# Kernel optimization log

Hardware: AMD Instinct MI355X
Metric: run time of the kernel (lower is better)

Reference implementation:

```python
import jax, jax.numpy as jnp
import numpy as np

B, S, D, H = 4, 2048, 1024, 16
HD = D // H  # head_dim = 64


def setup_inputs() -> dict:
    key = jax.random.key(0)
    ks = jax.random.split(key, 4)
    scale = 0.02
    return {
        "x": jax.random.normal(ks[0], (B, S, D), dtype=jnp.float32),
        "W_attn": jax.random.normal(ks[1], (D, 3 * D), dtype=jnp.float32) * scale,
        "b_attn": jnp.zeros((3 * D,), dtype=jnp.float32),
        "W_proj": jax.random.normal(ks[2], (D, D), dtype=jnp.float32) * scale,
        "b_proj": jnp.zeros((D,), dtype=jnp.float32),
    }


def reference(x, W_attn, b_attn, W_proj, b_proj):
    b, s, d = x.shape
    qkv = x @ W_attn + b_attn                      # [b, s, 3d]
    q, k, v = jnp.split(qkv, 3, axis=2)
    # [b, s, d] -> [b, h, s, hd]
    def to_heads(t):
        return t.reshape(b, s, H, HD).transpose(0, 2, 1, 3)
    q, k, v = to_heads(q), to_heads(k), to_heads(v)
    scores = jnp.einsum("bhqd,bhkd->bhqk", q, k) / jnp.sqrt(jnp.float32(HD))
    causal = jnp.tril(jnp.ones((s, s), dtype=bool))  # [s, s]
    scores = jnp.where(causal[None, None], scores, jnp.float32(-jnp.inf))
    probs = jax.nn.softmax(scores, axis=-1)
    y = jnp.einsum("bhqk,bhkd->bhqd", probs, v)    # [b, h, s, hd]
    y = y.transpose(0, 2, 1, 3).reshape(b, s, d)
    return y @ W_proj + b_proj
```

## Files before the change

kernel.cpp:

```cpp
#include <hip/hip_runtime.h>
#include <hip/hip_bf16.h>
#include <type_traits>

#define SQ    2048
#define DIM   1024
#define NH    16
#define HDIM  64
#define BATCH 4

typedef unsigned short u16;
typedef __bf16 bf16x8 __attribute__((ext_vector_type(8)));
typedef float  f32x4  __attribute__((ext_vector_type(4)));
typedef u16    u16x8  __attribute__((ext_vector_type(8)));

#define QSCALE 0.180336880f

__device__ __forceinline__ u16 f2bf(float f) {
  union { float f; unsigned u; } v; v.f = f;
  unsigned r = v.u + 0x7fffu + ((v.u >> 16) & 1u);
  return (u16)(r >> 16);
}

__device__ __forceinline__ float fast_exp2(float x) {
#if __has_builtin(__builtin_amdgcn_exp2f)
  return __builtin_amdgcn_exp2f(x);
#else
  float y;
  asm("v_exp_f32 %0, %1" : "=v"(y) : "v"(x));
  return y;
#endif
}

__device__ __forceinline__ void gll16(const u16* g, u16* l) {
  __builtin_amdgcn_global_load_lds((const __attribute__((address_space(1))) void*)g,
                                   (__attribute__((address_space(3))) void*)l,
                                   16, 0, 0);
}

__global__ __launch_bounds__(256)
void f32_to_bf16_vec(const float* __restrict__ in, u16* __restrict__ out, int n4)
{
  const int i = blockIdx.x * blockDim.x + threadIdx.x;
  if (i < n4) {
    const float4 v = ((const float4*)in)[i];
    ushort4 o;
    o.x = f2bf(v.x); o.y = f2bf(v.y); o.z = f2bf(v.z); o.w = f2bf(v.w);
    ((ushort4*)out)[i] = o;
  }
}

__global__ void transpose_f32_bf16(const float* __restrict__ in, u16* __restrict__ out,
                                   int R, int C)
{
  __shared__ u16 tile[32][33];
  const int bx = blockIdx.x * 32, by = blockIdx.y * 32;
  const int tx = threadIdx.x, ty = threadIdx.y;
  #pragma unroll
  for (int i = 0; i < 32; i += 8)
    tile[ty + i][tx] = f2bf(in[(size_t)(by + ty + i) * C + bx + tx]);
  __syncthreads();
  #pragma unroll
  for (int i = 0; i < 32; i += 8)
    out[(size_t)(bx + ty + i) * R + by + tx] = tile[tx][ty + i];
}

template<int MODE>
__global__ __launch_bounds__(256)
void gemm_bt(const u16* __restrict__ A, const u16* __restrict__ Bt,
             const float* __restrict__ bias, int K,
             u16* __restrict__ o0, u16* __restrict__ o1, float* __restrict__ of)
{
  __shared__ __align__(16) u16 A0[128 * 32], A1[128 * 32];
  __shared__ __align__(16) u16 B0[128 * 32], B1[128 * 32];

  const int t    = threadIdx.x;
  const int lane = t & 63, wave = t >> 6;
  const int l15  = lane & 15, quad = lane >> 4;
  const int wm   = (wave & 1) * 64, wn = (wave >> 1) * 64;
  const int m0   = blockIdx.y * 128, n0 = blockIdx.x * 128;

  const int srow = wave * 32 + (lane >> 2);
  const int scol = (lane & 3) * 8;

  f32x4 acc[4][4] = {};

  for (int k0 = 0; k0 < K; k0 += 64) {
    const u16* ga = A  + (size_t)(m0 + srow) * K + k0 + scol;
    const u16* gb = Bt + (size_t)(n0 + srow) * K + k0 + scol;
    gll16(ga,              &A0[(wave * 32)      * 32]);
    gll16(ga + 32,         &A1[(wave * 32)      * 32]);
    gll16(ga + 16 * K,     &A0[(wave * 32 + 16) * 32]);
    gll16(ga + 16 * K + 32,&A1[(wave * 32 + 16) * 32]);
    gll16(gb,              &B0[(wave * 32)      * 32]);
    gll16(gb + 32,         &B1[(wave * 32)      * 32]);
    gll16(gb + 16 * K,     &B0[(wave * 32 + 16) * 32]);
    gll16(gb + 16 * K + 32,&B1[(wave * 32 + 16) * 32]);
    __syncthreads();

    #pragma unroll
    for (int ks = 0; ks < 2; ++ks) {
      const u16* Als = ks ? A1 : A0;
      const u16* Bls = ks ? B1 : B0;
      bf16x8 af[4], bfr[4];
      #pragma unroll
      for (int i = 0; i < 4; ++i) af[i]  = *(const bf16x8*)&Als[(wm + 16*i + l15) * 32 + quad * 8];
      #pragma unroll
      for (int j = 0; j < 4; ++j) bfr[j] = *(const bf16x8*)&Bls[(wn + 16*j + l15) * 32 + quad * 8];
      #pragma unroll
      for (int i = 0; i < 4; ++i)
        #pragma unroll
        for (int j = 0; j < 4; ++j)
          acc[i][j] = (MODE == 2)
            ? __builtin_amdgcn_mfma_f32_16x16x32_bf16(bfr[j], af[i], acc[i][j], 0, 0, 0)
            : __builtin_amdgcn_mfma_f32_16x16x32_bf16(af[i], bfr[j], acc[i][j], 0, 0, 0);
    }
    __syncthreads();
  }

  if (MODE == 2) {
    #pragma unroll
    for (int j = 0; j < 4; ++j) {
      #pragma unroll
      for (int r = 0; r < 4; ++r) {
        const int d = n0 + wn + 16*j + quad * 4 + r;
        const float bn = bias[d];
        const int h = d >> 6, hd = d & 63;
        #pragma unroll
        for (int i = 0; i < 4; ++i) {
          const int m = m0 + wm + 16*i + l15;
          const int b = m >> 11, s = m & 2047;
          o0[(((size_t)(b * NH + h)) * HDIM + hd) * SQ + s] = f2bf(acc[i][j][r] + bn);
        }
      }
    }
  } else {
    #pragma unroll
    for (int j = 0; j < 4; ++j) {
      const int n = n0 + wn + 16*j + l15;
      const float bn = bias[n];
      #pragma unroll
      for (int i = 0; i < 4; ++i) {
        #pragma unroll
        for (int r = 0; r < 4; ++r) {
          const int m = m0 + wm + 16*i + quad * 4 + r;
          const float val = acc[i][j][r] + bn;
          if (MODE == 1) {
            const int sec = n >> 10, d = n & 1023;
            const int h = d >> 6, hd = d & 63;
            const int b = m >> 11, s = m & 2047;
            const int bh = b * NH + h;
            if (sec == 0) o0[((size_t)bh * SQ + s) * HDIM + hd] = f2bf(val * QSCALE);
            else          o1[((size_t)bh * SQ + s) * HDIM + hd] = f2bf(val);
          } else {
            of[(size_t)m * DIM + n] = val;
          }
        }
      }
    }
  }
}

template<int MODE>
__global__ __launch_bounds__(512)
void gemm256(const u16* __restrict__ A, const u16* __restrict__ Bt,
             const float* __restrict__ bias, int K,
             u16* __restrict__ o0, u16* __restrict__ o1, float* __restrict__ of)
{
  __shared__ __align__(16) u16 Als[2][256 * 64];
  __shared__ __align__(16) u16 Bls[2][256 * 64];

  const int t    = threadIdx.x;
  const int lane = t & 63, wave = t >> 6;
  const int l15  = lane & 15, quad = lane >> 4;
  const int wm   = (wave >> 2) * 128;
  const int wn   = (wave & 3) * 64;

  const int nwg  = gridDim.x * gridDim.y;
  const int orig = blockIdx.y * gridDim.x + blockIdx.x;
  const int swz  = (orig & 7) * (nwg >> 3) + (orig >> 3);
  const int bx   = swz % gridDim.x, by = swz / gridDim.x;
  const int m0   = by * 256, n0 = bx * 256;

  const int rx  = l15 & 7;
  const int cS0 = ((quad       ^ rx) << 3);
  const int cS1 = (((quad | 4) ^ rx) << 3);

  const int r3 = lane >> 3, c8 = lane & 7;
  const int scol = ((c8 ^ r3) << 3);

  const u16* gA = A  + (size_t)(m0 + wave * 8 + r3) * K + scol;
  const u16* gB = Bt + (size_t)(n0 + wave * 8 + r3) * K + scol;
  const size_t pstride = (size_t)64 * K;

  f32x4 acc[8][4] = {};

  auto stA = [&](int k0, int buf, int p) {
    gll16(gA + (size_t)p * pstride + k0, &Als[buf][(p * 64 + wave * 8) * 64]);
  };
  auto stB = [&](int k0, int buf, int p) {
    gll16(gB + (size_t)p * pstride + k0, &Bls[buf][(p * 64 + wave * 8) * 64]);
  };

  stA(0, 0, 0); stA(0, 0, 2); stB(0, 0, 0); stB(0, 0, 1);
  stB(0, 0, 2); stB(0, 0, 3); stA(0, 0, 1); stA(0, 0, 3);
  asm volatile("s_waitcnt vmcnt(2)" ::: "memory");
  __builtin_amdgcn_s_barrier();
  __builtin_amdgcn_sched_barrier(0);

  const int NT = K >> 6;
  for (int tt = 0; tt < NT; ++tt) {
    const int cur = tt & 1, nxt = cur ^ 1;
    const int k1  = (tt + 1) << 6;
    const bool st = (tt + 1 < NT);
    const u16* Ab = &Als[cur][0];
    const u16* Bb = &Bls[cur][0];
    bf16x8 af[4], bf0[4], bf1[4];

    #pragma unroll
    for (int nj = 0; nj < 4; ++nj)
      bf0[nj] = *(const bf16x8*)&Bb[(wn + 16 * nj + l15) * 64 + cS0];
    #pragma unroll
    for (int mi = 0; mi < 4; ++mi)
      af[mi] = *(const bf16x8*)&Ab[(wm + 16 * mi + l15) * 64 + cS0];
    if (st) { stA(k1, nxt, 0); stA(k1, nxt, 2); stB(k1, nxt, 0); stB(k1, nxt, 1); }
    __builtin_amdgcn_s_barrier();
    __builtin_amdgcn_s_setprio(1);
    #pragma unroll
    for (int mi = 0; mi < 4; ++mi)
      #pragma unroll
      for (int nj = 0; nj < 4; ++nj)
        acc[mi][nj] = (MODE == 2)
          ? __builtin_amdgcn_mfma_f32_16x16x32_bf16(bf0[nj], af[mi], acc[mi][nj], 0, 0, 0)
          : __builtin_amdgcn_mfma_f32_16x16x32_bf16(af[mi], bf0[nj], acc[mi][nj], 0, 0, 0);
    __builtin_amdgcn_s_setprio(0);
    if (st) asm volatile("s_waitcnt vmcnt(4)" ::: "memory");
    else    asm volatile("s_waitcnt vmcnt(0)" ::: "memory");
    __builtin_amdgcn_s_barrier();
    __builtin_amdgcn_sched_barrier(0);

    #pragma unroll
    for (int mi = 0; mi < 4; ++mi)
      af[mi] = *(const bf16x8*)&Ab[(wm + 64 + 16 * mi + l15) * 64 + cS0];
    if (st) { stB(k1, nxt, 2); stB(k1, nxt, 3); stA(k1, nxt, 1); stA(k1, nxt, 3); }
    __builtin_amdgcn_s_barrier();
    __builtin_amdgcn_s_setprio(1);
    #pragma unroll
    for (int mi = 0; mi < 4; ++mi)
      #pragma unroll
      for (int nj = 0; nj < 4; ++nj)
        acc[4 + mi][nj] = (MODE == 2)
          ? __builtin_amdgcn_mfma_f32_16x16x32_bf16(bf0[nj], af[mi], acc[4 + mi][nj], 0, 0, 0)
          : __builtin_amdgcn_mfma_f32_16x16x32_bf16(af[mi], bf0[nj], acc[4 + mi][nj], 0, 0, 0);
    __builtin_amdgcn_s_setprio(0);
    __builtin_amdgcn_s_barrier();

    #pragma unroll
    for (int nj = 0; nj < 4; ++nj)
      bf1[nj] = *(const bf16x8*)&Bb[(wn + 16 * nj + l15) * 64 + cS1];
    #pragma unroll
    for (int mi = 0; mi < 4; ++mi)
      af[mi] = *(const bf16x8*)&Ab[(wm + 16 * mi + l15) * 64 + cS1];
    __builtin_amdgcn_s_barrier();
    __builtin_amdgcn_s_setprio(1);
    #pragma unroll
    for (int mi = 0; mi < 4; ++mi)
      #pragma unroll
      for (int nj = 0; nj < 4; ++nj)
        acc[mi][nj] = (MODE == 2)
          ? __builtin_amdgcn_mfma_f32_16x16x32_bf16(bf1[nj], af[mi], acc[mi][nj], 0, 0, 0)
          : __builtin_amdgcn_mfma_f32_16x16x32_bf16(af[mi], bf1[nj], acc[mi][nj], 0, 0, 0);
    __builtin_amdgcn_s_setprio(0);
    __builtin_amdgcn_s_barrier();

    #pragma unroll
    for (int mi = 0; mi < 4; ++mi)
      af[mi] = *(const bf16x8*)&Ab[(wm + 64 + 16 * mi + l15) * 64 + cS1];
    __builtin_amdgcn_s_barrier();
    __builtin_amdgcn_s_setprio(1);
    #pragma unroll
    for (int mi = 0; mi < 4; ++mi)
      #pragma unroll
      for (int nj = 0; nj < 4; ++nj)
        acc[4 + mi][nj] = (MODE == 2)
          ? __builtin_amdgcn_mfma_f32_16x16x32_bf16(bf1[nj], af[mi], acc[4 + mi][nj], 0, 0, 0)
          : __builtin_amdgcn_mfma_f32_16x16x32_bf16(af[mi], bf1[nj], acc[4 + mi][nj], 0, 0, 0);
    __builtin_amdgcn_s_setprio(0);
    if (st) asm volatile("s_waitcnt vmcnt(2)" ::: "memory");
    __builtin_amdgcn_s_barrier();
    __builtin_amdgcn_sched_barrier(0);
  }

  if (MODE == 2) {
    #pragma unroll
    for (int j = 0; j < 4; ++j) {
      #pragma unroll
      for (int r = 0; r < 4; ++r) {
        const int d = n0 + wn + 16 * j + quad * 4 + r;
        const float bn = bias[d];
        const int h = d >> 6, hd = d & 63;
        #pragma unroll
        for (int i = 0; i < 8; ++i) {
          const int m = m0 + wm + 16 * i + l15;
          const int b = m >> 11, s = m & 2047;
          o0[(((size_t)(b * NH + h)) * HDIM + hd) * SQ + s] = f2bf(acc[i][j][r] + bn);
        }
      }
    }
  } else {
    #pragma unroll
    for (int j = 0; j < 4; ++j) {
      const int n = n0 + wn + 16 * j + l15;
      const float bn = bias[n];
      #pragma unroll
      for (int i = 0; i < 8; ++i) {
        #pragma unroll
        for (int r = 0; r < 4; ++r) {
          const int m = m0 + wm + 16 * i + quad * 4 + r;
          const float val = acc[i][j][r] + bn;
          if (MODE == 1) {
            const int sec = n >> 10, d = n & 1023;
            const int h = d >> 6, hd = d & 63;
            const int b = m >> 11, s = m & 2047;
            const int bh = b * NH + h;
            if (sec == 0) o0[((size_t)bh * SQ + s) * HDIM + hd] = f2bf(val * QSCALE);
            else          o1[((size_t)bh * SQ + s) * HDIM + hd] = f2bf(val);
          } else {
            of[(size_t)m * DIM + n] = val;
          }
        }
      }
    }
  }
}

__global__ __launch_bounds__(256, 2)
void attn_fused(const u16* __restrict__ q_ws, const u16* __restrict__ k_ws,
                const u16* __restrict__ v_t, u16* __restrict__ y_ws)
{
  __shared__ __align__(16) u16 Kls[3][64 * 64];
  __shared__ __align__(16) u16 Vls[3][64 * 64];
  __shared__ __align__(16) u16 Pls[4][64 * 64];

  const int bh = blockIdx.x;
  const int p  = blockIdx.y;
  const int b = bh >> 4, h = bh & 15;
  const int t = threadIdx.x;
  const int lane = t & 63, wave = t >> 6;
  const int l15 = lane & 15, quad = lane >> 4;
  const int rx  = l15 & 7;
  const int cK0 = ((quad      ^ rx) << 3);
  const int cK1 = (((quad | 4) ^ rx) << 3);
  const int pswz = rx << 3;

  const u16* Q  = q_ws + (size_t)bh * SQ * HDIM;
  const u16* Kp = k_ws + (size_t)bh * SQ * HDIM;
  const u16* Vp = v_t  + (size_t)bh * HDIM * SQ;

  const int qtH = 15 - p, qtL = p;
  const int qrowH = qtH * 128 + wave * 32;
  const int qrowL = qtL * 128 + wave * 32;

  bf16x8 qf[4][2];
  #pragma unroll
  for (int s = 0; s < 4; ++s) {
    const int qrow = ((s < 2) ? qrowH : qrowL) + 16 * (s & 1);
    #pragma unroll
    for (int ks = 0; ks < 2; ++ks)
      qf[s][ks] = *(const bf16x8*)&Q[(size_t)(qrow + l15) * HDIM + ks * 32 + quad * 8];
  }

  f32x4 o[4][4] = {};
  float l_q[4] = {};

  const int r3   = lane >> 3;
  const int c8   = lane & 7;
  const int scol = ((c8 ^ r3) << 3);

  auto stage = [&](int kv0, int buf) {
    gll16(&Kp[(size_t)(kv0 + wave*16     + r3) * HDIM + scol], &Kls[buf][(wave*16    ) * 64]);
    gll16(&Kp[(size_t)(kv0 + wave*16 + 8 + r3) * HDIM + scol], &Kls[buf][(wave*16 + 8) * 64]);
    gll16(&Vp[(size_t)(wave*16     + r3) * SQ + kv0 + scol],   &Vls[buf][(wave*16    ) * 64]);
    gll16(&Vp[(size_t)(wave*16 + 8 + r3) * SQ + kv0 + scol],   &Vls[buf][(wave*16 + 8) * 64]);
  };

  auto compute = [&](int kv0, int buf, auto doLc, auto mHc, auto mLc) {
    constexpr bool DO_L = decltype(doLc)::value;
    constexpr bool MH   = decltype(mHc)::value;
    constexpr bool ML   = decltype(mLc)::value;
    constexpr int  NS   = DO_L ? 4 : 2;
    f32x4 st[4][4] = {};
    const u16* Kb = Kls[buf];
    __builtin_amdgcn_s_setprio(1);
    #pragma unroll
    for (int ks = 0; ks < 2; ++ks) {
      const int cs = ks ? cK1 : cK0;
      #pragma unroll
      for (int kt = 0; kt < 4; ++kt) {
        bf16x8 kf = *(const bf16x8*)&Kb[(16*kt + l15) * 64 + cs];
        #pragma unroll
        for (int s = 0; s < NS; ++s)
          st[s][kt] = __builtin_amdgcn_mfma_f32_16x16x32_bf16(kf, qf[s][ks], st[s][kt], 0, 0, 0);
      }
    }
    __builtin_amdgcn_s_setprio(0);

    #pragma unroll
    for (int s = 0; s < NS; ++s) {
      const bool msk = (s < 2) ? MH : ML;
      const int qrow = ((s < 2) ? qrowH : qrowL) + 16 * (s & 1);
      const int q = qrow + l15;
      float rsum = 0.f;
      #pragma unroll
      for (int kt = 0; kt < 4; ++kt)
        #pragma unroll
        for (int r = 0; r < 4; ++r) {
          float pv = fast_exp2(st[s][kt][r]);
          if (msk && (kv0 + 16*kt + quad*4 + r) > q) pv = 0.f;
          st[s][kt][r] = pv;
          rsum += pv;
        }
      l_q[s] += rsum;
    }

    #pragma unroll
    for (int s = 0; s < NS; ++s)
      #pragma unroll
      for (int kt = 0; kt < 4; ++kt) {
        union { __hip_bfloat162 h2[2]; ushort4 u4; } pk;
        pk.h2[0] = __float22bfloat162_rn(make_float2(st[s][kt][0], st[s][kt][1]));
        pk.h2[1] = __float22bfloat162_rn(make_float2(st[s][kt][2], st[s][kt][3]));
        *(ushort4*)&Pls[wave][(16*s + l15) * 64 + ((16*kt + quad*4) ^ pswz)] = pk.u4;
      }

    const u16* Vb = Vls[buf];
    __builtin_amdgcn_s_setprio(1);
    #pragma unroll
    for (int ks = 0; ks < 2; ++ks) {
      const int cs = ks ? cK1 : cK0;
      bf16x8 vf[4];
      #pragma unroll
      for (int n = 0; n < 4; ++n)
        vf[n] = *(const bf16x8*)&Vb[(16*n + l15) * 64 + cs];
      #pragma unroll
      for (int s = 0; s < NS; ++s) {
        bf16x8 pa = *(const bf16x8*)&Pls[wave][(16*s + l15) * 64 + ((ks*32 + quad*8) ^ pswz)];
        #pragma unroll
        for (int n = 0; n < 4; ++n)
          o[s][n] = __builtin_amdgcn_mfma_f32_16x16x32_bf16(pa, vf[n], o[s][n], 0, 0, 0);
      }
    }
    __builtin_amdgcn_s_setprio(0);
  };

  const int ntiles = 2 * qtH + 2;
  const int lastH  = 2 * qtH + (wave >> 1);
  const int lastL  = 2 * qtL + (wave >> 1);

  using Fc = std::integral_constant<bool, false>;
  using Tc = std::integral_constant<bool, true>;

  stage(0, 0);
  stage(64, 1);

  int cur = 0;
  for (int kvt = 0; kvt < ntiles; ++kvt) {
    const int kv0 = kvt * 64;
    if (kvt + 1 < ntiles) asm volatile("s_waitcnt vmcnt(4)" ::: "memory");
    else                  asm volatile("s_waitcnt vmcnt(0)" ::: "memory");
    __builtin_amdgcn_s_barrier();
    __builtin_amdgcn_sched_barrier(0);
    if (kvt + 2 < ntiles) {
      int nb = cur + 2; if (nb >= 3) nb -= 3;
      stage((kvt + 2) * 64, nb);
    }
    if      (kvt <  lastL) compute(kv0, cur, Tc{}, Fc{}, Fc{});
    else if (kvt == lastL) compute(kv0, cur, Tc{}, Fc{}, Tc{});
    else if (kvt <  lastH) compute(kv0, cur, Fc{}, Fc{}, Fc{});
    else if (kvt == lastH) compute(kv0, cur, Fc{}, Tc{}, Fc{});
    if (++cur == 3) cur = 0;
  }

  #pragma unroll
  for (int s = 0; s < 4; ++s) {
    l_q[s] += __shfl_xor(l_q[s], 16);
    l_q[s] += __shfl_xor(l_q[s], 32);
  }
  #pragma unroll
  for (int s = 0; s < 4; ++s) {
    const int qrow = ((s < 2) ? qrowH : qrowL) + 16 * (s & 1);
    #pragma unroll
    for (int r = 0; r < 4; ++r) {
      const float lr = __shfl(l_q[s], quad * 4 + r);
      const float inv = 1.0f / lr;
      const int qg = qrow + quad * 4 + r;
      #pragma unroll
      for (int n = 0; n < 4; ++n)
        y_ws[((size_t)b * SQ + qg) * DIM + h * HDIM + 16*n + l15] = f2bf(o[s][n][r] * inv);
    }
  }
}

extern "C" void kernel_launch(void* const* d_in, const int* in_sizes, int n_in,
                              void* d_out, int out_size, void* d_ws, size_t ws_size,
                              hipStream_t stream)
{
  const float* x      = (const float*)d_in[0];
  const float* W_attn = (const float*)d_in[1];
  const float* b_attn = (const float*)d_in[2];
  const float* W_proj = (const float*)d_in[3];
  const float* b_proj = (const float*)d_in[4];
  float* out = (float*)d_out;

  char* ws = (char*)d_ws;
  u16* WattnT = (u16*)(ws);
  u16* WprojT = (u16*)(ws + 6291456);
  u16* xb     = (u16*)(ws + 8388608);
  u16* y_ws   = xb;
  u16* q_ws   = (u16*)(ws + 25165824);
  u16* k_ws   = (u16*)(ws + 41943040);
  u16* v_tw   = (u16*)(ws + 58720256);

  const dim3 tb(32, 8);
  transpose_f32_bf16<<<dim3(3 * DIM / 32, DIM / 32), tb, 0, stream>>>(W_attn, WattnT, DIM, 3 * DIM);
  transpose_f32_bf16<<<dim3(DIM / 32, DIM / 32), tb, 0, stream>>>(W_proj, WprojT, DIM, DIM);
  f32_to_bf16_vec<<<(BATCH * SQ * DIM / 4 + 255) / 256, 256, 0, stream>>>(x, xb, BATCH * SQ * DIM / 4);

  gemm256<1><<<dim3(2 * DIM / 256, BATCH * SQ / 256), 512, 0, stream>>>(
      xb, WattnT, b_attn, DIM, q_ws, k_ws, nullptr);
  gemm_bt<2><<<dim3(DIM / 128, BATCH * SQ / 128), 256, 0, stream>>>(
      xb, WattnT + (size_t)2048 * DIM, b_attn + 2048, DIM, v_tw, nullptr, nullptr);

  attn_fused<<<dim3(BATCH * NH, 8), 256, 0, stream>>>(q_ws, k_ws, v_tw, y_ws);

  gemm_bt<0><<<dim3(DIM / 128, BATCH * SQ / 128), 256, 0, stream>>>(
      y_ws, WprojT, b_proj, DIM, nullptr, nullptr, out);
}
```

Baseline: 251.2 us.

## Replace V and output projection GEMMs with 256x128 double-buffered pipelined kernel

```diff
diff --git a/kernel.cpp b/kernel.cpp
--- a/kernel.cpp
+++ b/kernel.cpp
@@ -333,6 +333,164 @@
   }
 }
 
+template<int MODE>
+__global__ __launch_bounds__(512)
+void gemm128n(const u16* __restrict__ A, const u16* __restrict__ Bt,
+              const float* __restrict__ bias, int K,
+              u16* __restrict__ o0, float* __restrict__ of)
+{
+  __shared__ __align__(16) u16 Als[2][256 * 64];
+  __shared__ __align__(16) u16 Bls[2][128 * 64];
+
+  const int t    = threadIdx.x;
+  const int lane = t & 63, wave = t >> 6;
+  const int l15  = lane & 15, quad = lane >> 4;
+  const int wm   = (wave >> 2) * 128;
+  const int wn   = (wave & 3) * 32;
+  const int m0   = blockIdx.y * 256, n0 = blockIdx.x * 128;
+
+  const int rx  = l15 & 7;
+  const int cS0 = ((quad       ^ rx) << 3);
+  const int cS1 = (((quad | 4) ^ rx) << 3);
+
+  const int r3 = lane >> 3, c8 = lane & 7;
+  const int scol = ((c8 ^ r3) << 3);
+
+  const u16* gA = A  + (size_t)(m0 + wave * 8 + r3) * K + scol;
+  const u16* gB = Bt + (size_t)(n0 + wave * 8 + r3) * K + scol;
+  const size_t pstride = (size_t)64 * K;
+
+  f32x4 acc[8][2] = {};
+
+  auto stA = [&](int k0, int buf, int p) {
+    gll16(gA + (size_t)p * pstride + k0, &Als[buf][(p * 64 + wave * 8) * 64]);
+  };
+  auto stB = [&](int k0, int buf, int p) {
+    gll16(gB + (size_t)p * pstride + k0, &Bls[buf][(p * 64 + wave * 8) * 64]);
+  };
+
+  stA(0, 0, 0); stA(0, 0, 2); stB(0, 0, 0); stB(0, 0, 1);
+  stA(0, 0, 1); stA(0, 0, 3);
+  asm volatile("s_waitcnt vmcnt(2)" ::: "memory");
+  __builtin_amdgcn_s_barrier();
+  __builtin_amdgcn_sched_barrier(0);
+
+  const int NT = K >> 6;
+  for (int tt = 0; tt < NT; ++tt) {
+    const int cur = tt & 1, nxt = cur ^ 1;
+    const int k1  = (tt + 1) << 6;
+    const bool st = (tt + 1 < NT);
+    const u16* Ab = &Als[cur][0];
+    const u16* Bb = &Bls[cur][0];
+    bf16x8 af[4], bf0[2], bf1[2];
+
+    #pragma unroll
+    for (int nj = 0; nj < 2; ++nj)
+      bf0[nj] = *(const bf16x8*)&Bb[(wn + 16 * nj + l15) * 64 + cS0];
+    #pragma unroll
+    for (int mi = 0; mi < 4; ++mi)
+      af[mi] = *(const bf16x8*)&Ab[(wm + 16 * mi + l15) * 64 + cS0];
+    if (st) { stA(k1, nxt, 0); stA(k1, nxt, 2); stB(k1, nxt, 0); }
+    __builtin_amdgcn_s_barrier();
+    __builtin_amdgcn_s_setprio(1);
+    #pragma unroll
+    for (int mi = 0; mi < 4; ++mi)
+      #pragma unroll
+      for (int nj = 0; nj < 2; ++nj)
+        acc[mi][nj] = (MODE == 2)
+          ? __builtin_amdgcn_mfma_f32_16x16x32_bf16(bf0[nj], af[mi], acc[mi][nj], 0, 0, 0)
+          : __builtin_amdgcn_mfma_f32_16x16x32_bf16(af[mi], bf0[nj], acc[mi][nj], 0, 0, 0);
+    __builtin_amdgcn_s_setprio(0);
+    if (st) asm volatile("s_waitcnt vmcnt(3)" ::: "memory");
+    else    asm volatile("s_waitcnt vmcnt(0)" ::: "memory");
+    __builtin_amdgcn_s_barrier();
+    __builtin_amdgcn_sched_barrier(0);
+
+    #pragma unroll
+    for (int mi = 0; mi < 4; ++mi)
+      af[mi] = *(const bf16x8*)&Ab[(wm + 64 + 16 * mi + l15) * 64 + cS0];
+    if (st) { stB(k1, nxt, 1); stA(k1, nxt, 1); stA(k1, nxt, 3); }
+    __builtin_amdgcn_s_barrier();
+    __builtin_amdgcn_s_setprio(1);
+    #pragma unroll
+    for (int mi = 0; mi < 4; ++mi)
+      #pragma unroll
+      for (int nj = 0; nj < 2; ++nj)
+        acc[4 + mi][nj] = (MODE == 2)
+          ? __builtin_amdgcn_mfma_f32_16x16x32_bf16(bf0[nj], af[mi], acc[4 + mi][nj], 0, 0, 0)
+          : __builtin_amdgcn_mfma_f32_16x16x32_bf16(af[mi], bf0[nj], acc[4 + mi][nj], 0, 0, 0);
+    __builtin_amdgcn_s_setprio(0);
+    __builtin_amdgcn_s_barrier();
+
+    #pragma unroll
+    for (int nj = 0; nj < 2; ++nj)
+      bf1[nj] = *(const bf16x8*)&Bb[(wn + 16 * nj + l15) * 64 + cS1];
+    #pragma unroll
+    for (int mi = 0; mi < 4; ++mi)
+      af[mi] = *(const bf16x8*)&Ab[(wm + 16 * mi + l15) * 64 + cS1];
+    __builtin_amdgcn_s_barrier();
+    __builtin_amdgcn_s_setprio(1);
+    #pragma unroll
+    for (int mi = 0; mi < 4; ++mi)
+      #pragma unroll
+      for (int nj = 0; nj < 2; ++nj)
+        acc[mi][nj] = (MODE == 2)
+          ? __builtin_amdgcn_mfma_f32_16x16x32_bf16(bf1[nj], af[mi], acc[mi][nj], 0, 0, 0)
+          : __builtin_amdgcn_mfma_f32_16x16x32_bf16(af[mi], bf1[nj], acc[mi][nj], 0, 0, 0);
+    __builtin_amdgcn_s_setprio(0);
+    __builtin_amdgcn_s_barrier();
+
+    #pragma unroll
+    for (int mi = 0; mi < 4; ++mi)
+      af[mi] = *(const bf16x8*)&Ab[(wm + 64 + 16 * mi + l15) * 64 + cS1];
+    __builtin_amdgcn_s_barrier();
+    __builtin_amdgcn_s_setprio(1);
+    #pragma unroll
+    for (int mi = 0; mi < 4; ++mi)
+      #pragma unroll
+      for (int nj = 0; nj < 2; ++nj)
+        acc[4 + mi][nj] = (MODE == 2)
+          ? __builtin_amdgcn_mfma_f32_16x16x32_bf16(bf1[nj], af[mi], acc[4 + mi][nj], 0, 0, 0)
+          : __builtin_amdgcn_mfma_f32_16x16x32_bf16(af[mi], bf1[nj], acc[4 + mi][nj], 0, 0, 0);
+    __builtin_amdgcn_s_setprio(0);
+    if (st) asm volatile("s_waitcnt vmcnt(2)" ::: "memory");
+    __builtin_amdgcn_s_barrier();
+    __builtin_amdgcn_sched_barrier(0);
+  }
+
+  if (MODE == 2) {
+    #pragma unroll
+    for (int j = 0; j < 2; ++j) {
+      #pragma unroll
+      for (int r = 0; r < 4; ++r) {
+        const int d = n0 + wn + 16 * j + quad * 4 + r;
+        const float bn = bias[d];
+        const int h = d >> 6, hd = d & 63;
+        #pragma unroll
+        for (int i = 0; i < 8; ++i) {
+          const int m = m0 + wm + 16 * i + l15;
+          const int b = m >> 11, s = m & 2047;
+          o0[(((size_t)(b * NH + h)) * HDIM + hd) * SQ + s] = f2bf(acc[i][j][r] + bn);
+        }
+      }
+    }
+  } else {
+    #pragma unroll
+    for (int j = 0; j < 2; ++j) {
+      const int n = n0 + wn + 16 * j + l15;
+      const float bn = bias[n];
+      #pragma unroll
+      for (int i = 0; i < 8; ++i) {
+        #pragma unroll
+        for (int r = 0; r < 4; ++r) {
+          const int m = m0 + wm + 16 * i + quad * 4 + r;
+          of[(size_t)m * DIM + n] = acc[i][j][r] + bn;
+        }
+      }
+    }
+  }
+}
+
 __global__ __launch_bounds__(256, 2)
 void attn_fused(const u16* __restrict__ q_ws, const u16* __restrict__ k_ws,
                 const u16* __restrict__ v_t, u16* __restrict__ y_ws)
@@ -527,11 +685,11 @@
 
   gemm256<1><<<dim3(2 * DIM / 256, BATCH * SQ / 256), 512, 0, stream>>>(
       xb, WattnT, b_attn, DIM, q_ws, k_ws, nullptr);
-  gemm_bt<2><<<dim3(DIM / 128, BATCH * SQ / 128), 256, 0, stream>>>(
-      xb, WattnT + (size_t)2048 * DIM, b_attn + 2048, DIM, v_tw, nullptr, nullptr);
+  gemm128n<2><<<dim3(DIM / 128, BATCH * SQ / 256), 512, 0, stream>>>(
+      xb, WattnT + (size_t)2048 * DIM, b_attn + 2048, DIM, v_tw, nullptr);
 
   attn_fused<<<dim3(BATCH * NH, 8), 256, 0, stream>>>(q_ws, k_ws, v_tw, y_ws);
 
-  gemm_bt<0><<<dim3(DIM / 128, BATCH * SQ / 128), 256, 0, stream>>>(
-      y_ws, WprojT, b_proj, DIM, nullptr, nullptr, out);
-}
+  gemm128n<0><<<dim3(DIM / 128, BATCH * SQ / 256), 512, 0, stream>>>(
+      y_ws, WprojT, b_proj, DIM, nullptr, out);
+}
```

Result: slower. 257.6 us (+2.5%).
